# Optimization experiments

Hardware: AMD Instinct MI355X
Metric: run time of the kernel (lower is better)

Reference implementation:

```python
import jax, jax.numpy as jnp
import numpy as np

DN = ('NCHW', 'OIHW', 'NCHW')
NUM_DOMAINS = 4


def conv2d(x, w, pad, groups=1):
    return jax.lax.conv_general_dilated(x, w, (1, 1), pad, dimension_numbers=DN,
                                        feature_group_count=groups)


def batchnorm2d(x, w, b, eps=1e-3):
    m = x.mean(axis=(0, 2, 3), keepdims=True)
    v = x.var(axis=(0, 2, 3), keepdims=True)
    return (x - m) / jnp.sqrt(v + eps) * w[None, :, None, None] + b[None, :, None, None]


def avgpool_w(x, k):
    B, C, H, W = x.shape
    Wo = W // k
    return x[..., :Wo * k].reshape(B, C, H, Wo, k).mean(axis=-1)


def mink(u, v):
    # Minkowski inner product <u,v>_L = -u0*v0 + <us,vs>
    return -u[..., 0] * v[..., 0] + (u[..., 1:] * v[..., 1:]).sum(-1)


def lorentz_elu(x):
    s = jax.nn.elu(x[..., 1:])
    t = jnp.sqrt(1.0 + (s * s).sum(-1, keepdims=True))
    return jnp.concatenate([t, s], -1)


def lorentz_avgpool_w(x, k):
    # (B,H,W,C) Lorentz points; window mean then Lorentz centroid projection
    B, H, W, C = x.shape
    Wo = W // k
    s = x[:, :, :Wo * k].reshape(B, H, Wo, k, C).mean(axis=3)
    d = jnp.sqrt(jnp.clip(jnp.abs(mink(s, s)), 1e-8, None))[..., None]
    return s / d


def lorentz_dbn(x, domains, beta, gamma, eps=1e-5):
    # Domain-specific Riemannian batch norm on the Lorentz manifold (k=1),
    # scalar dispersion (Frechet-mean centroid + geodesic variance per domain).
    B, H, W, C = x.shape
    pts = x.reshape(B, H * W, C)
    npts = float(H * W)
    s = jax.ops.segment_sum(pts.sum(axis=1), domains, num_segments=NUM_DOMAINS)  # (D,C)
    cnt = jax.ops.segment_sum(jnp.full((B,), npts, x.dtype), domains, num_segments=NUM_DOMAINS)
    cnt = jnp.maximum(cnt, 1.0)
    s = s / cnt[:, None]
    mu = s / jnp.sqrt(jnp.clip(jnp.abs(mink(s, s)), 1e-8, None))[:, None]  # (D,C) centroids
    mu_b = mu[domains][:, None, :]                                         # (B,1,C)
    ip = mink(mu_b, pts)                                                   # (B,HW)
    dist = jnp.arccosh(jnp.clip(-ip, 1.0 + 1e-7, None))
    u = pts + ip[..., None] * mu_b
    un = jnp.sqrt(jnp.clip(mink(u, u), 1e-8, None))
    v = dist[..., None] * u / un[..., None]                                # log_mu(x)
    var = jax.ops.segment_sum((dist ** 2).sum(axis=1), domains, num_segments=NUM_DOMAINS) / cnt
    o = jnp.zeros((C,), x.dtype).at[0].set(1.0)
    # parallel transport mu -> origin
    v = v + (-v[..., :1]) / (1.0 + mu_b[..., :1]) * (mu_b + o)
    # rescale by gamma / sqrt(var)
    v = v * (gamma / jnp.sqrt(var[domains] + eps))[:, None, None]
    # parallel transport origin -> beta, then expmap at beta
    v = v + (mink(beta, v) / (1.0 + beta[0]))[..., None] * (o + beta)
    vn = jnp.sqrt(jnp.clip(mink(v, v), 1e-8, None))[..., None]
    y = jnp.cosh(vn) * beta + jnp.sinh(vn) * v / vn
    return y.reshape(B, H, W, C)


def setup_inputs() -> dict:
    key = jax.random.key(0)
    ks = jax.random.split(key, 12)
    B = 128
    d = {}
    d['x'] = jax.random.normal(ks[0], (B, 32, 1024), jnp.float32)
    d['domains'] = jax.random.randint(ks[1], (B,), 0, NUM_DOMAINS, jnp.int32)
    d['conv1_w'] = 0.1 * jax.random.normal(ks[2], (16, 1, 1, 32), jnp.float32)
    d['bn1_w'] = jnp.ones((16,), jnp.float32)
    d['bn1_b'] = jnp.zeros((16,), jnp.float32)
    d['dw_w'] = 0.1 * jax.random.normal(ks[3], (32, 1, 32, 1), jnp.float32)
    d['bn2_w'] = jnp.ones((32,), jnp.float32)
    d['bn2_b'] = jnp.zeros((32,), jnp.float32)
    d['ec1_w'] = 0.1 * jax.random.normal(ks[4], (32, 1, 1, 16), jnp.float32)
    d['b2c1_w'] = 0.1 * jax.random.normal(ks[5], (32, 1, 1, 16), jnp.float32)
    d['b2c2_w'] = 0.1 * jax.random.normal(ks[6], (32, 32, 1, 1), jnp.float32)
    d['bn3_w'] = jnp.ones((32,), jnp.float32)
    d['bn3_b'] = jnp.zeros((32,), jnp.float32)
    d['lc1_w'] = 0.2 * jax.random.normal(ks[7], (33, 33), jnp.float32)
    d['bn_beta'] = jnp.zeros((33,), jnp.float32).at[0].set(1.0)
    d['bn_gamma'] = jnp.ones((1,), jnp.float32)
    d['mlr_a'] = 0.1 * jax.random.normal(ks[8], (1,), jnp.float32)
    d['mlr_z'] = 0.1 * jax.random.normal(ks[9], (1, 512), jnp.float32)
    return d


def reference(x, domains, conv1_w, bn1_w, bn1_b, dw_w, bn2_w, bn2_b, ec1_w,
              b2c1_w, b2c2_w, bn3_w, bn3_b, lc1_w, bn_beta, bn_gamma, mlr_a, mlr_z):
    h = x[:, None]                                       # (B,1,32,1024)
    # block1: temporal conv + BN + depthwise spatial conv + BN + ELU + pool
    h = conv2d(h, conv1_w, ((0, 0), (16, 16)))           # (B,16,32,1025)
    h = batchnorm2d(h, bn1_w, bn1_b)
    h = conv2d(h, dw_w, ((0, 0), (0, 0)), groups=16)     # (B,32,1,1025)
    h = batchnorm2d(h, bn2_w, bn2_b)
    h = jax.nn.elu(h)
    h = avgpool_w(h, 4)                                  # (B,32,1,256)
    # ec1 + block2
    h = conv2d(h, ec1_w, ((0, 0), (8, 8)), groups=32)    # (B,32,1,257)
    h = conv2d(h, b2c1_w, ((0, 0), (8, 8)), groups=32)   # (B,32,1,258)
    h = conv2d(h, b2c2_w, ((0, 0), (0, 0)))              # (B,32,1,258)
    h = batchnorm2d(h, bn3_w, bn3_b)
    h = jax.nn.elu(h)
    h = avgpool_w(h, 4)                                  # (B,32,1,64)
    # to Lorentz: permute, L2-normalize, pad time, projx (time = sqrt(1+|s|^2))
    h = jnp.transpose(h, (0, 2, 3, 1))                   # (B,1,64,32)
    h = h / jnp.clip(jnp.linalg.norm(h, axis=-1, keepdims=True), 1e-12, None)
    t = jnp.sqrt(1.0 + (h * h).sum(-1, keepdims=True))
    h = jnp.concatenate([t, h], -1)                      # (B,1,64,33)
    # LorentzConv2d kernel 1 == Lorentz fully-connected: linear then recompute time
    y = jnp.einsum('bhwc,oc->bhwo', h, lc1_w)
    ys = y[..., 1:]
    yt = jnp.sqrt(1.0 + (ys * ys).sum(-1, keepdims=True))
    h = jnp.concatenate([yt, ys], -1)                    # (B,1,64,33)
    h = lorentz_dbn(h, domains, bn_beta, bn_gamma)
    h = lorentz_elu(h)
    h = lorentz_avgpool_w(h, 4)                          # (B,1,16,33)
    # lorentz_flatten: concat spaces, recompute time -> (B, 16*32+1)
    B = h.shape[0]
    fs = h[..., 1:].reshape(B, -1)
    ft = jnp.sqrt(1.0 + (fs * fs).sum(-1, keepdims=True))
    features = jnp.concatenate([ft, fs], -1)             # (B,513)
    # Lorentz MLR (k=1)
    norm_z = jnp.linalg.norm(mlr_z, axis=-1)             # (1,)
    w_t = jnp.sinh(mlr_a) * norm_z
    bet = jnp.sqrt(jnp.clip(-w_t ** 2 + (jnp.cosh(mlr_a) * norm_z) ** 2, 1e-8, None))
    alpha = -w_t * features[:, :1] + jnp.cosh(mlr_a) * (features[:, 1:] @ mlr_z.T)
    dd = jnp.abs(jnp.arcsinh(alpha / bet))
    logits = jnp.sign(alpha) * bet * dd                  # (B,1)
    return logits.squeeze(-1), features
```

## Files before the change

### kernel.cpp

```cpp
#include <hip/hip_runtime.h>
#include <math.h>

#define Bn 128
#define Hh 32
#define Wx 1024

#define N1f 4198400.0f
#define N2f 131200.0f
#define N3f 33024.0f

#define OFF_EH     33
#define OFF_ET     48
#define OFF_G      64
#define OFF_G2     544
#define OFF_A1     1024
#define OFF_B1     1040
#define OFF_S1_3   1056
#define OFF_S2_3   1088
#define OFF_SEG    1120
#define OFF_CNT    1252
#define OFF_DSQ    1256
#define ZERO_N     1280
#define OFF_PC     2048
#define OFF_PS     34816
#define OFF_PD1    35840
#define OFF_PD2    68608
#define OFF_DWOUT  101376
#define OFF_E2     (101376 + 4194304)
#define OFF_C3     OFF_DWOUT
#define OFF_PTS    (OFF_C3 + 1056768)
#define OFF_VO     (OFF_PTS + 270336)

__device__ __forceinline__ float eluf(float x) { return x > 0.f ? x : expm1f(x); }

__global__ __launch_bounds__(256) void k_edge(const float* __restrict__ x,
                                              float* __restrict__ ws) {
    __shared__ float hd[64 * 48];
    __shared__ float tl[64 * 48];
    int tid = threadIdx.x;
    int r0 = blockIdx.x * 64;
    for (int i = tid; i < 64 * 32; i += 256) {
        int r = i >> 5, c = i & 31;
        tl[r * 48 + 16 + c] = 0.f;
    }
#pragma unroll
    for (int it = 0; it < 4; it++) {
        int idx = tid + it * 256;
        int r = idx >> 4, q = idx & 15;
        const float4* base = (const float4*)(x + (r0 + r) * Wx);
        if (q < 12) ((float4*)(hd + r * 48))[q] = base[q];
        else        ((float4*)(tl + r * 48))[q - 12] = base[252 + (q - 12)];
    }
    __syncthreads();
    for (int p = tid; p < 990; p += 256) {
        float acc = 0.f;
        if (p < 480) {
            int d = p / 15, j = p - d * 15;
            for (int r = 0; r < 64; r++) acc += hd[r * 48 + j] * hd[r * 48 + j + d];
            atomicAdd(&ws[OFF_G + p], acc);
        } else if (p < 960) {
            int p2 = p - 480;
            int d = p2 / 15, j = p2 - d * 15;
            for (int r = 0; r < 64; r++) acc += tl[r * 48 + 1 + j] * tl[r * 48 + 1 + j + d];
            atomicAdd(&ws[OFF_G2 + p2], acc);
        } else {
            int j = p - 960;
            if (j < 15) { for (int r = 0; r < 64; r++) acc += hd[r * 48 + j]; }
            else        { for (int r = 0; r < 64; r++) acc += tl[r * 48 + 1 + (j - 15)]; }
            atomicAdd(&ws[OFF_EH + j], acc);
        }
    }
}

__global__ __launch_bounds__(256, 1) void k_corr(const float* __restrict__ x,
                                                 float* __restrict__ ws) {
    __shared__ float xs[2][1060];
    __shared__ float cacc[32];
    __shared__ float sacc;
    int tid = threadIdx.x;
    if (tid < 32) cacc[tid] = 0.f;
    if (tid == 32) sacc = 0.f;
    for (int i = 1024 + tid; i < 1060; i += 256) { xs[0][i] = 0.f; xs[1][i] = 0.f; }
    float acc[32];
#pragma unroll
    for (int d = 0; d < 32; d++) acc[d] = 0.f;
    float sp = 0.f;
    int r0 = blockIdx.x * 4;
    ((float4*)xs[0])[tid] = ((const float4*)(x + r0 * Wx))[tid];
    __syncthreads();
    for (int rr = 0; rr < 4; rr++) {
        float4 nxt;
        if (rr < 3) nxt = ((const float4*)(x + (r0 + rr + 1) * Wx))[tid];
        const float* bq = xs[rr & 1];
        float v[36];
#pragma unroll
        for (int q = 0; q < 9; q++) {
            float4 t4 = ((const float4*)bq)[tid + q];
            v[4 * q] = t4.x; v[4 * q + 1] = t4.y; v[4 * q + 2] = t4.z; v[4 * q + 3] = t4.w;
        }
#pragma unroll
        for (int i = 0; i < 4; i++) {
            sp += v[i];
#pragma unroll
            for (int d = 0; d < 32; d++) acc[d] += v[i] * v[i + d];
        }
        if (rr < 3) ((float4*)xs[(rr + 1) & 1])[tid] = nxt;
        __syncthreads();
    }
    int lane = tid & 63;
#pragma unroll
    for (int d = 0; d < 32; d++) {
        float vv = acc[d];
#pragma unroll
        for (int off = 32; off > 0; off >>= 1) vv += __shfl_down(vv, off);
        if (lane == 0) atomicAdd(&cacc[d], vv);
    }
    {
        float vv = sp;
#pragma unroll
        for (int off = 32; off > 0; off >>= 1) vv += __shfl_down(vv, off);
        if (lane == 0) atomicAdd(&sacc, vv);
    }
    __syncthreads();
    if (tid < 32) ws[OFF_PC + tid * 1024 + blockIdx.x] = cacc[tid];
    if (tid == 32) ws[OFF_PS + blockIdx.x] = sacc;
}

__global__ __launch_bounds__(512) void k_fold(const float* __restrict__ w1,
                                              const float* __restrict__ bn1w,
                                              const float* __restrict__ bn1b,
                                              float* __restrict__ ws) {
    __shared__ float PH[32][16];
    __shared__ float PT[32][16];
    __shared__ float Ts[32];
    __shared__ float w1s[512];
    __shared__ float sumsq[16];
    __shared__ float meanv[16];
    __shared__ float Cs[32];
    __shared__ float sS[16];
    int tid = threadIdx.x;
    w1s[tid] = w1[tid];
    if (tid < 16) sumsq[tid] = 0.f;
    {
        int d = tid >> 4, i = tid & 15;
        const float4* pc = (const float4*)(ws + OFF_PC + d * 1024 + i * 64);
        float s = 0.f;
#pragma unroll
        for (int k = 0; k < 16; k++) { float4 t4 = pc[k]; s += t4.x + t4.y + t4.z + t4.w; }
        s += __shfl_down(s, 8); s += __shfl_down(s, 4);
        s += __shfl_down(s, 2); s += __shfl_down(s, 1);
        if (i == 0) Cs[d] = s;
    }
    __syncthreads();
    if (tid < 32) {
        int d = tid;
        float s = 0.f;
        for (int j = 0; j < 15; j++) { s += ws[OFF_G + d * 15 + j]; PH[d][j] = s; }
        float s2 = 0.f;
        for (int j = 14; j >= 0; j--) { s2 += ws[OFF_G2 + d * 15 + j]; PT[d][j] = s2; }
    } else if (tid < 48) {
        int i = tid - 32;
        const float4* ps = (const float4*)(ws + OFF_PS + i * 64);
        float s = 0.f;
#pragma unroll
        for (int k = 0; k < 16; k++) { float4 t4 = ps[k]; s += t4.x + t4.y + t4.z + t4.w; }
        sS[i] = s;
    }
    __syncthreads();
    if (tid >= 64 && tid < 96) {
        int k = tid - 64;
        float S = 0.f;
        for (int j = 0; j < 16; j++) S += sS[j];
        float t = S;
        for (int j = 0; j <= k - 17; j++) t -= ws[OFF_EH + j];
        if (k <= 14) for (int j = k; j < 15; j++) t -= ws[OFF_ET + j];
        Ts[k] = t;
    }
    __syncthreads();
    int c = tid >> 5, d = tid & 31;
    float Cd = Cs[d];
    float part = 0.f;
    for (int k = 0; k + d < 32; k++) {
        float head = (k >= 17) ? PH[d][k - 17] : 0.f;
        float tail = (k <= 14) ? PT[d][k] : 0.f;
        float R = Cd - head - tail;
        part += w1s[c * 32 + k] * w1s[c * 32 + k + d] * R;
    }
    if (d > 0) part *= 2.f;
    atomicAdd(&sumsq[c], part);
    if (d == 0) {
        float mp = 0.f;
        for (int k = 0; k < 32; k++) mp += w1s[c * 32 + k] * Ts[k];
        meanv[c] = mp / N1f;
    }
    __syncthreads();
    if (tid < 16) {
        float mean = meanv[tid];
        float var = fmaxf(sumsq[tid] / N1f - mean * mean, 0.f);
        float a = bn1w[tid] / sqrtf(var + 1e-3f);
        ws[OFF_A1 + tid] = a;
        ws[OFF_B1 + tid] = bn1b[tid] - mean * a;
    }
}

__global__ __launch_bounds__(256, 2) void k_dw(const float* __restrict__ x,
                                               const float* __restrict__ w1,
                                               const float* __restrict__ dww,
                                               float* __restrict__ ws) {
    __shared__ float buf[32 * 160];
    __shared__ float dws[1024];
    __shared__ float w1s[512];
    __shared__ float a1s[16], b1s[16], Dv[32];
    int tid = threadIdx.x;
    int b = blockIdx.x;
    int z = blockIdx.y;
    int wt0 = z * 128;
    for (int i = tid; i < 1024; i += 256) dws[i] = dww[i];
    w1s[tid] = w1[tid];
    w1s[256 + tid] = w1[256 + tid];
    if (tid < 16) { a1s[tid] = ws[OFF_A1 + tid]; b1s[tid] = ws[OFF_B1 + tid]; }
    const float* xb = x + b * (Hh * Wx);
    for (int i = tid; i < 32 * 160; i += 256) {
        int h = i / 160, cc = i - h * 160;
        int gc = wt0 - 16 + cc;
        buf[i] = (gc >= 0 && gc < Wx) ? xb[h * Wx + gc] : 0.f;
    }
    __syncthreads();
    if (tid < 32) {
        float d = 0.f;
        for (int h = 0; h < 32; h++) d += dws[tid * 32 + h];
        Dv[tid] = d;
    }
    float acc[32];
    if (tid < 160) {
        float xv[32];
#pragma unroll
        for (int h = 0; h < 32; h++) xv[h] = buf[h * 160 + tid];
#pragma unroll
        for (int oc = 0; oc < 32; oc++) acc[oc] = 0.f;
#pragma unroll
        for (int h = 0; h < 32; h++) {
#pragma unroll
            for (int oc = 0; oc < 32; oc++) acc[oc] += xv[h] * dws[oc * 32 + h];
        }
    }
    __syncthreads();
    if (tid < 160) {
#pragma unroll
        for (int oc = 0; oc < 32; oc++) buf[oc * 160 + tid] = acc[oc];
    }
    __syncthreads();
    int lane = tid & 63;
    int wave = tid >> 6;
    int half = lane >> 5;
    int qw = lane & 31;
    for (int pass = 0; pass < 4; pass++) {
        int oc = pass * 8 + wave * 2 + half;
        int g = oc >> 1;
        float wr[32];
        const float4* wg = (const float4*)(w1s + g * 32);
#pragma unroll
        for (int q = 0; q < 8; q++) {
            float4 t4 = wg[q];
            wr[4 * q] = t4.x; wr[4 * q + 1] = t4.y; wr[4 * q + 2] = t4.z; wr[4 * q + 3] = t4.w;
        }
        float ag = a1s[g], bb = b1s[g] * Dv[oc];
        float y[36];
        const float4* yq = (const float4*)(buf + oc * 160 + 4 * qw);
#pragma unroll
        for (int q = 0; q < 9; q++) {
            float4 t4 = yq[q];
            y[4 * q] = t4.x; y[4 * q + 1] = t4.y; y[4 * q + 2] = t4.z; y[4 * q + 3] = t4.w;
        }
        float ls1 = 0.f, ls2 = 0.f;
        float ov[4];
#pragma unroll
        for (int m = 0; m < 4; m++) {
            float s = 0.f;
#pragma unroll
            for (int k = 0; k < 32; k++) s += wr[k] * y[m + k];
            float val = ag * s + bb;
            ov[m] = val;
            ls1 += val; ls2 += val * val;
        }
        *((float4*)(ws + OFF_DWOUT + (b * 32 + oc) * 1024 + wt0 + 4 * qw)) =
            make_float4(ov[0], ov[1], ov[2], ov[3]);
        if (z == 7 && qw == 0) {
            float s = 0.f;
#pragma unroll
            for (int k = 0; k < 32; k++) s += wr[k] * buf[oc * 160 + 128 + k];
            float val = ag * s + bb;
            ls1 += val; ls2 += val * val;
        }
#pragma unroll
        for (int off = 16; off > 0; off >>= 1) {
            ls1 += __shfl_down(ls1, off, 32);
            ls2 += __shfl_down(ls2, off, 32);
        }
        if (qw == 0) {
            ws[OFF_PD1 + oc * 1024 + z * 128 + b] = ls1;
            ws[OFF_PD2 + oc * 1024 + z * 128 + b] = ls2;
        }
    }
}

__global__ __launch_bounds__(64) void k_pe(const float* __restrict__ ec1w,
                                           const float* __restrict__ bc1w,
                                           const float* __restrict__ bn2w,
                                           const float* __restrict__ bn2b,
                                           float* __restrict__ ws) {
    __shared__ float ins[272];
    __shared__ float e1p[288];
    int b = blockIdx.x, c = blockIdx.y;
    int t = threadIdx.x;
    if (t < 8) { ins[t] = 0.f; ins[264 + t] = 0.f; e1p[t] = 0.f; }
    if (t < 23) e1p[265 + t] = 0.f;
    const float4* p1 = (const float4*)(ws + OFF_PD1 + c * 1024);
    const float4* p2 = (const float4*)(ws + OFF_PD2 + c * 1024);
    float s1 = 0.f, s2 = 0.f;
#pragma unroll
    for (int q = 0; q < 4; q++) {
        float4 a4 = p1[t * 4 + q];
        float4 c4 = p2[t * 4 + q];
        s1 += a4.x + a4.y + a4.z + a4.w;
        s2 += c4.x + c4.y + c4.z + c4.w;
    }
#pragma unroll
    for (int off = 32; off > 0; off >>= 1) {
        s1 += __shfl_xor(s1, off);
        s2 += __shfl_xor(s2, off);
    }
    float mean = s1 / N2f;
    float var = fmaxf(s2 / N2f - mean * mean, 0.f);
    float a = bn2w[c] / sqrtf(var + 1e-3f);
    float bb = bn2b[c] - mean * a;
    const float4* dr = (const float4*)(ws + OFF_DWOUT + (b * 32 + c) * 1024);
#pragma unroll
    for (int q = 0; q < 4; q++) {
        float4 v4 = dr[q * 64 + t];
        ins[8 + q * 64 + t] = 0.25f * (eluf(a * v4.x + bb) + eluf(a * v4.y + bb) +
                                       eluf(a * v4.z + bb) + eluf(a * v4.w + bb));
    }
    __syncthreads();
    float ek[16], bk[16];
#pragma unroll
    for (int k = 0; k < 16; k++) { ek[k] = ec1w[c * 16 + k]; bk[k] = bc1w[c * 16 + k]; }
    for (int w = t; w < 257; w += 64) {
        float s = 0.f;
#pragma unroll
        for (int k = 0; k < 16; k++) s += ins[w + k] * ek[k];
        e1p[8 + w] = s;
    }
    __syncthreads();
    float* e2r = ws + OFF_E2 + (b * 32 + c) * 258;
    for (int w = t; w < 258; w += 64) {
        float s = 0.f;
#pragma unroll
        for (int k = 0; k < 16; k++) s += e1p[w + k] * bk[k];
        e2r[w] = s;
    }
}

__global__ __launch_bounds__(256) void k_sep2(const float* __restrict__ bc2w,
                                              float* __restrict__ ws) {
    __shared__ float es[32 * 129];
    __shared__ float bs[1056];
    int b = blockIdx.x;
    int wb = blockIdx.y * 129;
    int t = threadIdx.x;
    for (int i = t; i < 1024; i += 256) { int o = i >> 5, cc = i & 31; bs[o * 33 + cc] = bc2w[i]; }
    const float* e2b = ws + OFF_E2 + b * 8256;
    for (int i = t; i < 4128; i += 256) {
        int cc = i / 129, wl = i - cc * 129;
        es[i] = e2b[cc * 258 + wb + wl];
    }
    __syncthreads();
    int o = t >> 3, w0 = t & 7;
    float wr[32];
#pragma unroll
    for (int cc = 0; cc < 32; cc++) wr[cc] = bs[o * 33 + cc];
    float s1 = 0.f, s2 = 0.f;
    float* c3r = ws + OFF_C3 + (b * 32 + o) * 258 + wb;
    for (int wl = w0; wl < 129; wl += 8) {
        float s = 0.f;
#pragma unroll
        for (int cc = 0; cc < 32; cc++) s += es[cc * 129 + wl] * wr[cc];
        c3r[wl] = s;
        s1 += s; s2 += s * s;
    }
    s1 += __shfl_down(s1, 4, 8); s1 += __shfl_down(s1, 2, 8); s1 += __shfl_down(s1, 1, 8);
    s2 += __shfl_down(s2, 4, 8); s2 += __shfl_down(s2, 2, 8); s2 += __shfl_down(s2, 1, 8);
    if (w0 == 0) {
        atomicAdd(&ws[OFF_S1_3 + o], s1);
        atomicAdd(&ws[OFF_S2_3 + o], s2);
    }
}

__global__ __launch_bounds__(256, 1) void k_head(const float* __restrict__ bn3w,
                                                 const float* __restrict__ bn3b,
                                                 const float* __restrict__ lc1w,
                                                 const int* __restrict__ domains,
                                                 float* __restrict__ ws) {
    __shared__ float q[2048];
    __shared__ float lc1s[1089];
    __shared__ float psum[33];
    __shared__ float ssyp[4][64];
    __shared__ float a3s[32], b3s[32];
    int tid = threadIdx.x;
    int b = blockIdx.x;
    if (tid < 32) {
        float mean = ws[OFF_S1_3 + tid] / N3f;
        float var = fmaxf(ws[OFF_S2_3 + tid] / N3f - mean * mean, 0.f);
        float a = bn3w[tid] / sqrtf(var + 1e-3f);
        a3s[tid] = a;
        b3s[tid] = bn3b[tid] - mean * a;
    }
    for (int i = tid; i < 1089; i += 256) lc1s[i] = lc1w[i];
    __syncthreads();
    const float* c3 = ws + OFF_C3 + b * 8256;
    for (int idx = tid; idx < 2048; idx += 256) {
        int c = idx >> 6, wp = idx & 63;
        float a = a3s[c], bb = b3s[c];
        float acc = 0.f;
#pragma unroll
        for (int j = 0; j < 4; j++) {
            float e = a * c3[c * 258 + wp * 4 + j] + bb;
            acc += eluf(e);
        }
        q[idx] = 0.25f * acc;
    }
    __syncthreads();
    int w = tid & 63, sub = tid >> 6;
    float qv[32];
    float ssq = 0.f;
#pragma unroll
    for (int c = 0; c < 32; c++) { qv[c] = q[c * 64 + w]; ssq += qv[c] * qv[c]; }
    float inv = 1.f / fmaxf(sqrtf(ssq), 1e-12f);
    float ss2 = 0.f;
#pragma unroll
    for (int c = 0; c < 32; c++) { qv[c] *= inv; ss2 += qv[c] * qv[c]; }
    float t = sqrtf(1.f + ss2);
    int o0 = 1 + sub * 8;
    float p[8];
    float ssy_part = 0.f;
#pragma unroll
    for (int i = 0; i < 8; i++) {
        int o = o0 + i;
        float s = lc1s[o * 33] * t;
#pragma unroll
        for (int c = 0; c < 32; c++) s += lc1s[o * 33 + 1 + c] * qv[c];
        p[i] = s;
        ssy_part += s * s;
    }
    ssyp[sub][w] = ssy_part;
    float* pr = ws + OFF_PTS + (b * 64 + w) * 33;
#pragma unroll
    for (int i = 0; i < 8; i++) pr[o0 + i] = p[i];
    __syncthreads();
    float yt = 0.f;
    if (sub == 0) {
        float ssy = ssyp[0][w] + ssyp[1][w] + ssyp[2][w] + ssyp[3][w];
        yt = sqrtf(1.f + ssy);
        pr[0] = yt;
    }
#pragma unroll
    for (int i = 0; i < 8; i++) {
        float vv = p[i];
#pragma unroll
        for (int off = 32; off > 0; off >>= 1) vv += __shfl_down(vv, off);
        if (w == 0) psum[o0 + i] = vv;
    }
    {
        float vv = yt;
#pragma unroll
        for (int off = 32; off > 0; off >>= 1) vv += __shfl_down(vv, off);
        if (w == 0 && sub == 0) psum[0] = vv;
    }
    __syncthreads();
    int dom = domains[b];
    if (tid < 33) atomicAdd(&ws[OFF_SEG + dom * 33 + tid], psum[tid]);
    if (tid == 64) atomicAdd(&ws[OFF_CNT + dom], 64.f);
}

__global__ __launch_bounds__(64, 1) void k_tangent(const int* __restrict__ domains,
                                                   float* __restrict__ ws) {
    int b = blockIdx.x;
    int w = threadIdx.x;
    int dom = domains[b];
    float cnt = fmaxf(ws[OFF_CNT + dom], 1.f);
    float m[33];
    float s0 = ws[OFF_SEG + dom * 33] / cnt;
    m[0] = s0;
    float msum = 0.f;
#pragma unroll
    for (int c = 1; c < 33; c++) {
        m[c] = ws[OFF_SEG + dom * 33 + c] / cnt;
        msum += m[c] * m[c];
    }
    float mkm = -s0 * s0 + msum;
    float dn = 1.f / sqrtf(fmaxf(fabsf(mkm), 1e-8f));
#pragma unroll
    for (int c = 0; c < 33; c++) m[c] *= dn;
    const float* pr = ws + OFF_PTS + (b * 64 + w) * 33;
    float p[33];
#pragma unroll
    for (int c = 0; c < 33; c++) p[c] = pr[c];
    float ip = -m[0] * p[0];
#pragma unroll
    for (int c = 1; c < 33; c++) ip += m[c] * p[c];
    float z = fmaxf(-ip, 1.f + 1e-7f);
    float dist = acoshf(z);
    float u[33];
#pragma unroll
    for (int c = 0; c < 33; c++) u[c] = p[c] + ip * m[c];
    float mk = -u[0] * u[0];
#pragma unroll
    for (int c = 1; c < 33; c++) mk += u[c] * u[c];
    float un = sqrtf(fmaxf(mk, 1e-8f));
    float r = dist / un;
    float v0 = r * u[0];
    float coef = -v0 / (1.f + m[0]);
    float* vo = ws + OFF_VO + (b * 64 + w) * 33;
    vo[0] = v0 + coef * (m[0] + 1.f);
#pragma unroll
    for (int c = 1; c < 33; c++) vo[c] = r * u[c] + coef * m[c];
    float dsq = dist * dist;
#pragma unroll
    for (int off = 32; off > 0; off >>= 1) dsq += __shfl_down(dsq, off);
    if (w == 0) atomicAdd(&ws[OFF_DSQ + dom], dsq);
}

__global__ __launch_bounds__(64, 1) void k_final(const int* __restrict__ domains,
                                                 const float* __restrict__ beta,
                                                 const float* __restrict__ gamma,
                                                 const float* __restrict__ mlr_a,
                                                 const float* __restrict__ mlr_z,
                                                 float* __restrict__ ws,
                                                 float* __restrict__ out) {
    __shared__ float he[64 * 33];
    __shared__ float hp[16 * 33];
    int b = blockIdx.x;
    int w = threadIdx.x;
    int dom = domains[b];
    float cnt = fmaxf(ws[OFF_CNT + dom], 1.f);
    float var = ws[OFF_DSQ + dom] / cnt;
    float sc = gamma[0] / sqrtf(var + 1e-5f);
    float bt[33];
#pragma unroll
    for (int c = 0; c < 33; c++) bt[c] = beta[c];
    const float* vo = ws + OFF_VO + (b * 64 + w) * 33;
    float v[33];
#pragma unroll
    for (int c = 0; c < 33; c++) v[c] = vo[c] * sc;
    float mb = -bt[0] * v[0];
#pragma unroll
    for (int c = 1; c < 33; c++) mb += bt[c] * v[c];
    float coef = mb / (1.f + bt[0]);
    v[0] += coef * (1.f + bt[0]);
#pragma unroll
    for (int c = 1; c < 33; c++) v[c] += coef * bt[c];
    float mk = -v[0] * v[0];
#pragma unroll
    for (int c = 1; c < 33; c++) mk += v[c] * v[c];
    float vn = sqrtf(fmaxf(mk, 1e-8f));
    float ch = coshf(vn), sh = sinhf(vn) / vn;
    float ss = 0.f;
#pragma unroll
    for (int c = 1; c < 33; c++) {
        float y = ch * bt[c] + sh * v[c];
        float s = eluf(y);
        he[w * 33 + c] = s;
        ss += s * s;
    }
    he[w * 33] = sqrtf(1.f + ss);
    __syncthreads();
    if (w < 16) {
        float tmp[33];
        float mk2;
        {
            float a0 = 0.25f * (he[(4 * w) * 33] + he[(4 * w + 1) * 33] +
                                he[(4 * w + 2) * 33] + he[(4 * w + 3) * 33]);
            tmp[0] = a0;
            mk2 = -a0 * a0;
        }
#pragma unroll
        for (int c = 1; c < 33; c++) {
            float a = 0.25f * (he[(4 * w) * 33 + c] + he[(4 * w + 1) * 33 + c] +
                               he[(4 * w + 2) * 33 + c] + he[(4 * w + 3) * 33 + c]);
            tmp[c] = a;
            mk2 += a * a;
        }
        float dd = sqrtf(fmaxf(fabsf(mk2), 1e-8f));
#pragma unroll
        for (int c = 0; c < 33; c++) hp[w * 33 + c] = tmp[c] / dd;
    }
    __syncthreads();
    float ssq = 0.f, sdz = 0.f, zz = 0.f;
    for (int j = w; j < 512; j += 64) {
        float val = hp[(j >> 5) * 33 + 1 + (j & 31)];
        float zv = mlr_z[j];
        ssq += val * val;
        sdz += val * zv;
        zz += zv * zv;
        out[128 + b * 513 + 1 + j] = val;
    }
#pragma unroll
    for (int off = 32; off > 0; off >>= 1) {
        ssq += __shfl_down(ssq, off);
        sdz += __shfl_down(sdz, off);
        zz += __shfl_down(zz, off);
    }
    if (w == 0) {
        float nz = sqrtf(zz);
        float a = mlr_a[0];
        float cha = coshf(a);
        float wt = sinhf(a) * nz;
        float cn = cha * nz;
        float bet = sqrtf(fmaxf(cn * cn - wt * wt, 1e-8f));
        float ft = sqrtf(1.f + ssq);
        float alpha = -wt * ft + cha * sdz;
        out[128 + b * 513] = ft;
        out[b] = bet * asinhf(alpha / bet);
    }
}

extern "C" void kernel_launch(void* const* d_in, const int* in_sizes, int n_in,
                              void* d_out, int out_size, void* d_ws, size_t ws_size,
                              hipStream_t stream) {
    const float* x       = (const float*)d_in[0];
    const int*   domains = (const int*)d_in[1];
    const float* conv1_w = (const float*)d_in[2];
    const float* bn1_w   = (const float*)d_in[3];
    const float* bn1_b   = (const float*)d_in[4];
    const float* dw_w    = (const float*)d_in[5];
    const float* bn2_w   = (const float*)d_in[6];
    const float* bn2_b   = (const float*)d_in[7];
    const float* ec1_w   = (const float*)d_in[8];
    const float* b2c1_w  = (const float*)d_in[9];
    const float* b2c2_w  = (const float*)d_in[10];
    const float* bn3_w   = (const float*)d_in[11];
    const float* bn3_b   = (const float*)d_in[12];
    const float* lc1_w   = (const float*)d_in[13];
    const float* bn_beta = (const float*)d_in[14];
    const float* bn_gamma= (const float*)d_in[15];
    const float* mlr_a   = (const float*)d_in[16];
    const float* mlr_z   = (const float*)d_in[17];
    float* out = (float*)d_out;
    float* ws  = (float*)d_ws;

    hipMemsetAsync(ws, 0, ZERO_N * sizeof(float), stream);
    k_edge<<<64, 256, 0, stream>>>(x, ws);
    k_corr<<<1024, 256, 0, stream>>>(x, ws);
    k_fold<<<1, 512, 0, stream>>>(conv1_w, bn1_w, bn1_b, ws);
    k_dw<<<dim3(128, 8), 256, 0, stream>>>(x, conv1_w, dw_w, ws);
    k_pe<<<dim3(128, 32), 64, 0, stream>>>(ec1_w, b2c1_w, bn2_w, bn2_b, ws);
    k_sep2<<<dim3(128, 2), 256, 0, stream>>>(b2c2_w, ws);
    k_head<<<Bn, 256, 0, stream>>>(bn3_w, bn3_b, lc1_w, domains, ws);
    k_tangent<<<Bn, 64, 0, stream>>>(domains, ws);
    k_final<<<Bn, 64, 0, stream>>>(domains, bn_beta, bn_gamma, mlr_a, mlr_z, ws, out);
}
```

Before: 248.6 us.

## Widen k_dw width tile to 256 and read weights directly from global

The depthwise-conv kernel now covers 256 output columns per block instead of 128, halving the grid and shrinking the 16-column halo overhead. Weight tiles are no longer staged in shared memory but read as uniform float4 loads from global. Each wave handles a full 64-lane row per output channel, so the partial-sum layout shrinks and k_pe reads half as many partials. In exchange there are fewer blocks in flight and more shared memory per block, which may lower occupancy.

```diff
diff --git a/kernel.cpp b/kernel.cpp
--- a/kernel.cpp
+++ b/kernel.cpp
@@ -24,9 +24,9 @@
 #define OFF_PC     2048
 #define OFF_PS     34816
 #define OFF_PD1    35840
-#define OFF_PD2    68608
-#define OFF_DWOUT  101376
-#define OFF_E2     (101376 + 4194304)
+#define OFF_PD2    52224
+#define OFF_DWOUT  68608
+#define OFF_E2     (68608 + 4194304)
 #define OFF_C3     OFF_DWOUT
 #define OFF_PTS    (OFF_C3 + 1056768)
 #define OFF_VO     (OFF_PTS + 270336)
@@ -207,66 +207,64 @@
                                                const float* __restrict__ w1,
                                                const float* __restrict__ dww,
                                                float* __restrict__ ws) {
-    __shared__ float buf[32 * 160];
-    __shared__ float dws[1024];
-    __shared__ float w1s[512];
+    __shared__ float buf[32 * 288];
     __shared__ float a1s[16], b1s[16], Dv[32];
     int tid = threadIdx.x;
     int b = blockIdx.x;
     int z = blockIdx.y;
-    int wt0 = z * 128;
-    for (int i = tid; i < 1024; i += 256) dws[i] = dww[i];
-    w1s[tid] = w1[tid];
-    w1s[256 + tid] = w1[256 + tid];
+    int wt0 = z * 256;
     if (tid < 16) { a1s[tid] = ws[OFF_A1 + tid]; b1s[tid] = ws[OFF_B1 + tid]; }
+    else if (tid >= 32 && tid < 64) {
+        int oc = tid - 32;
+        float d = 0.f;
+        for (int h = 0; h < 32; h++) d += dww[oc * 32 + h];
+        Dv[oc] = d;
+    }
     const float* xb = x + b * (Hh * Wx);
-    for (int i = tid; i < 32 * 160; i += 256) {
-        int h = i / 160, cc = i - h * 160;
+    for (int i = tid; i < 32 * 288; i += 256) {
+        int h = i / 288, cc = i - h * 288;
         int gc = wt0 - 16 + cc;
         buf[i] = (gc >= 0 && gc < Wx) ? xb[h * Wx + gc] : 0.f;
     }
     __syncthreads();
-    if (tid < 32) {
-        float d = 0.f;
-        for (int h = 0; h < 32; h++) d += dws[tid * 32 + h];
-        Dv[tid] = d;
-    }
-    float acc[32];
-    if (tid < 160) {
+    for (int rep = 0; rep < 2; rep++) {
+        if (rep == 1 && tid >= 32) break;
+        int c = rep == 0 ? tid : 256 + tid;
         float xv[32];
 #pragma unroll
-        for (int h = 0; h < 32; h++) xv[h] = buf[h * 160 + tid];
-#pragma unroll
-        for (int oc = 0; oc < 32; oc++) acc[oc] = 0.f;
-#pragma unroll
-        for (int h = 0; h < 32; h++) {
-#pragma unroll
-            for (int oc = 0; oc < 32; oc++) acc[oc] += xv[h] * dws[oc * 32 + h];
-        }
-    }
-    __syncthreads();
-    if (tid < 160) {
-#pragma unroll
-        for (int oc = 0; oc < 32; oc++) buf[oc * 160 + tid] = acc[oc];
+        for (int h = 0; h < 32; h++) xv[h] = buf[h * 288 + c];
+        float acc[32];
+#pragma unroll
+        for (int oc = 0; oc < 32; oc++) {
+            const float4* dg = (const float4*)(dww + oc * 32);
+            float a = 0.f;
+#pragma unroll
+            for (int hq = 0; hq < 8; hq++) {
+                float4 d = dg[hq];
+                a += xv[4 * hq] * d.x + xv[4 * hq + 1] * d.y +
+                     xv[4 * hq + 2] * d.z + xv[4 * hq + 3] * d.w;
+            }
+            acc[oc] = a;
+        }
+#pragma unroll
+        for (int oc = 0; oc < 32; oc++) buf[oc * 288 + c] = acc[oc];
     }
     __syncthreads();
     int lane = tid & 63;
-    int wave = tid >> 6;
-    int half = lane >> 5;
-    int qw = lane & 31;
-    for (int pass = 0; pass < 4; pass++) {
-        int oc = pass * 8 + wave * 2 + half;
+    int wv = __builtin_amdgcn_readfirstlane(tid >> 6);
+    for (int pass = 0; pass < 8; pass++) {
+        int oc = pass * 4 + wv;
         int g = oc >> 1;
+        const float4* wg4 = (const float4*)(w1 + g * 32);
         float wr[32];
-        const float4* wg = (const float4*)(w1s + g * 32);
 #pragma unroll
         for (int q = 0; q < 8; q++) {
-            float4 t4 = wg[q];
+            float4 t4 = wg4[q];
             wr[4 * q] = t4.x; wr[4 * q + 1] = t4.y; wr[4 * q + 2] = t4.z; wr[4 * q + 3] = t4.w;
         }
         float ag = a1s[g], bb = b1s[g] * Dv[oc];
         float y[36];
-        const float4* yq = (const float4*)(buf + oc * 160 + 4 * qw);
+        const float4* yq = (const float4*)(buf + oc * 288 + 4 * lane);
 #pragma unroll
         for (int q = 0; q < 9; q++) {
             float4 t4 = yq[q];
@@ -283,23 +281,23 @@
             ov[m] = val;
             ls1 += val; ls2 += val * val;
         }
-        *((float4*)(ws + OFF_DWOUT + (b * 32 + oc) * 1024 + wt0 + 4 * qw)) =
+        *((float4*)(ws + OFF_DWOUT + (b * 32 + oc) * 1024 + wt0 + 4 * lane)) =
             make_float4(ov[0], ov[1], ov[2], ov[3]);
-        if (z == 7 && qw == 0) {
+        if (z == 3 && lane == 0) {
             float s = 0.f;
 #pragma unroll
-            for (int k = 0; k < 32; k++) s += wr[k] * buf[oc * 160 + 128 + k];
+            for (int k = 0; k < 32; k++) s += wr[k] * buf[oc * 288 + 256 + k];
             float val = ag * s + bb;
             ls1 += val; ls2 += val * val;
         }
 #pragma unroll
-        for (int off = 16; off > 0; off >>= 1) {
-            ls1 += __shfl_down(ls1, off, 32);
-            ls2 += __shfl_down(ls2, off, 32);
-        }
-        if (qw == 0) {
-            ws[OFF_PD1 + oc * 1024 + z * 128 + b] = ls1;
-            ws[OFF_PD2 + oc * 1024 + z * 128 + b] = ls2;
+        for (int off = 32; off > 0; off >>= 1) {
+            ls1 += __shfl_down(ls1, off);
+            ls2 += __shfl_down(ls2, off);
+        }
+        if (lane == 0) {
+            ws[OFF_PD1 + oc * 512 + z * 128 + b] = ls1;
+            ws[OFF_PD2 + oc * 512 + z * 128 + b] = ls2;
         }
     }
 }
@@ -315,16 +313,11 @@
     int t = threadIdx.x;
     if (t < 8) { ins[t] = 0.f; ins[264 + t] = 0.f; e1p[t] = 0.f; }
     if (t < 23) e1p[265 + t] = 0.f;
-    const float4* p1 = (const float4*)(ws + OFF_PD1 + c * 1024);
-    const float4* p2 = (const float4*)(ws + OFF_PD2 + c * 1024);
-    float s1 = 0.f, s2 = 0.f;
-#pragma unroll
-    for (int q = 0; q < 4; q++) {
-        float4 a4 = p1[t * 4 + q];
-        float4 c4 = p2[t * 4 + q];
-        s1 += a4.x + a4.y + a4.z + a4.w;
-        s2 += c4.x + c4.y + c4.z + c4.w;
-    }
+    const float4* p1 = (const float4*)(ws + OFF_PD1 + c * 512);
+    const float4* p2 = (const float4*)(ws + OFF_PD2 + c * 512);
+    float4 a0 = p1[t * 2], a1 = p1[t * 2 + 1], c0 = p2[t * 2], c1 = p2[t * 2 + 1];
+    float s1 = a0.x + a0.y + a0.z + a0.w + a1.x + a1.y + a1.z + a1.w;
+    float s2 = c0.x + c0.y + c0.z + c0.w + c1.x + c1.y + c1.z + c1.w;
 #pragma unroll
     for (int off = 32; off > 0; off >>= 1) {
         s1 += __shfl_xor(s1, off);
@@ -652,7 +645,7 @@
     k_edge<<<64, 256, 0, stream>>>(x, ws);
     k_corr<<<1024, 256, 0, stream>>>(x, ws);
     k_fold<<<1, 512, 0, stream>>>(conv1_w, bn1_w, bn1_b, ws);
-    k_dw<<<dim3(128, 8), 256, 0, stream>>>(x, conv1_w, dw_w, ws);
+    k_dw<<<dim3(128, 4), 256, 0, stream>>>(x, conv1_w, dw_w, ws);
     k_pe<<<dim3(128, 32), 64, 0, stream>>>(ec1_w, b2c1_w, bn2_w, bn2_b, ws);
     k_sep2<<<dim3(128, 2), 256, 0, stream>>>(b2c2_w, ws);
     k_head<<<Bn, 256, 0, stream>>>(bn3_w, bn3_b, lc1_w, domains, ws);
```

New measurement: 240.1 us. -3.4%, faster.

## Fuse pooled separable conv stages into one per-batch kernel, drop atomics

Applied to the files above, without the earlier changes.

Merges k_pe and k_sep2 into one kernel per batch item that keeps the intermediate e2 tensor in shared memory instead of writing it to global memory and reading it back. The BN3 statistics atomics are replaced by per-batch partial sums that k_head reduces itself. k_dw now loads x straight from global into registers, skipping the shared staging buffer and one barrier. The trade-off is that only 128 blocks run the fused stage instead of 4096 plus 256, which lowers parallelism and adds extra barriers per channel pass.

```diff
diff --git a/kernel.cpp b/kernel.cpp
--- a/kernel.cpp
+++ b/kernel.cpp
@@ -15,8 +15,6 @@
 #define OFF_G2     544
 #define OFF_A1     1024
 #define OFF_B1     1040
-#define OFF_S1_3   1056
-#define OFF_S2_3   1088
 #define OFF_SEG    1120
 #define OFF_CNT    1252
 #define OFF_DSQ    1256
@@ -25,9 +23,9 @@
 #define OFF_PS     34816
 #define OFF_PD1    35840
 #define OFF_PD2    68608
-#define OFF_DWOUT  101376
-#define OFF_E2     (101376 + 4194304)
-#define OFF_C3     OFF_DWOUT
+#define OFF_PB3    101376
+#define OFF_DWOUT  109568
+#define OFF_C3     (109568 + 4194304)
 #define OFF_PTS    (OFF_C3 + 1056768)
 #define OFF_VO     (OFF_PTS + 270336)
 
@@ -219,33 +217,32 @@
     w1s[tid] = w1[tid];
     w1s[256 + tid] = w1[256 + tid];
     if (tid < 16) { a1s[tid] = ws[OFF_A1 + tid]; b1s[tid] = ws[OFF_B1 + tid]; }
-    const float* xb = x + b * (Hh * Wx);
-    for (int i = tid; i < 32 * 160; i += 256) {
-        int h = i / 160, cc = i - h * 160;
-        int gc = wt0 - 16 + cc;
-        buf[i] = (gc >= 0 && gc < Wx) ? xb[h * Wx + gc] : 0.f;
-    }
     __syncthreads();
     if (tid < 32) {
         float d = 0.f;
         for (int h = 0; h < 32; h++) d += dws[tid * 32 + h];
         Dv[tid] = d;
     }
-    float acc[32];
     if (tid < 160) {
+        int gc = wt0 - 16 + tid;
+        bool inr = (gc >= 0 && gc < Wx);
+        const float* xb = x + b * (Hh * Wx) + gc;
         float xv[32];
 #pragma unroll
-        for (int h = 0; h < 32; h++) xv[h] = buf[h * 160 + tid];
-#pragma unroll
-        for (int oc = 0; oc < 32; oc++) acc[oc] = 0.f;
-#pragma unroll
-        for (int h = 0; h < 32; h++) {
-#pragma unroll
-            for (int oc = 0; oc < 32; oc++) acc[oc] += xv[h] * dws[oc * 32 + h];
-        }
-    }
-    __syncthreads();
-    if (tid < 160) {
+        for (int h = 0; h < 32; h++) xv[h] = inr ? xb[h << 10] : 0.f;
+        float acc[32];
+#pragma unroll
+        for (int oc = 0; oc < 32; oc++) {
+            const float4* dg = (const float4*)(dws + oc * 32);
+            float a = 0.f;
+#pragma unroll
+            for (int hq = 0; hq < 8; hq++) {
+                float4 d = dg[hq];
+                a += xv[4 * hq] * d.x + xv[4 * hq + 1] * d.y +
+                     xv[4 * hq + 2] * d.z + xv[4 * hq + 3] * d.w;
+            }
+            acc[oc] = a;
+        }
 #pragma unroll
         for (int oc = 0; oc < 32; oc++) buf[oc * 160 + tid] = acc[oc];
     }
@@ -304,95 +301,95 @@
     }
 }
 
-__global__ __launch_bounds__(64) void k_pe(const float* __restrict__ ec1w,
-                                           const float* __restrict__ bc1w,
-                                           const float* __restrict__ bn2w,
-                                           const float* __restrict__ bn2b,
-                                           float* __restrict__ ws) {
-    __shared__ float ins[272];
-    __shared__ float e1p[288];
-    int b = blockIdx.x, c = blockIdx.y;
+__global__ __launch_bounds__(256) void k_pesep(const float* __restrict__ ec1w,
+                                               const float* __restrict__ bc1w,
+                                               const float* __restrict__ bn2w,
+                                               const float* __restrict__ bn2b,
+                                               const float* __restrict__ bc2w,
+                                               float* __restrict__ ws) {
+    __shared__ float e2s[32 * 258];
+    __shared__ float ins[4][272];
+    __shared__ float e1p[4][288];
+    __shared__ float bs[1056];
+    __shared__ float a2s[32], b2s[32];
+    int b = blockIdx.x;
     int t = threadIdx.x;
-    if (t < 8) { ins[t] = 0.f; ins[264 + t] = 0.f; e1p[t] = 0.f; }
-    if (t < 23) e1p[265 + t] = 0.f;
-    const float4* p1 = (const float4*)(ws + OFF_PD1 + c * 1024);
-    const float4* p2 = (const float4*)(ws + OFF_PD2 + c * 1024);
-    float s1 = 0.f, s2 = 0.f;
-#pragma unroll
-    for (int q = 0; q < 4; q++) {
-        float4 a4 = p1[t * 4 + q];
-        float4 c4 = p2[t * 4 + q];
-        s1 += a4.x + a4.y + a4.z + a4.w;
-        s2 += c4.x + c4.y + c4.z + c4.w;
-    }
-#pragma unroll
-    for (int off = 32; off > 0; off >>= 1) {
-        s1 += __shfl_xor(s1, off);
-        s2 += __shfl_xor(s2, off);
-    }
-    float mean = s1 / N2f;
-    float var = fmaxf(s2 / N2f - mean * mean, 0.f);
-    float a = bn2w[c] / sqrtf(var + 1e-3f);
-    float bb = bn2b[c] - mean * a;
-    const float4* dr = (const float4*)(ws + OFF_DWOUT + (b * 32 + c) * 1024);
-#pragma unroll
-    for (int q = 0; q < 4; q++) {
-        float4 v4 = dr[q * 64 + t];
-        ins[8 + q * 64 + t] = 0.25f * (eluf(a * v4.x + bb) + eluf(a * v4.y + bb) +
-                                       eluf(a * v4.z + bb) + eluf(a * v4.w + bb));
-    }
-    __syncthreads();
-    float ek[16], bk[16];
-#pragma unroll
-    for (int k = 0; k < 16; k++) { ek[k] = ec1w[c * 16 + k]; bk[k] = bc1w[c * 16 + k]; }
-    for (int w = t; w < 257; w += 64) {
-        float s = 0.f;
-#pragma unroll
-        for (int k = 0; k < 16; k++) s += ins[w + k] * ek[k];
-        e1p[8 + w] = s;
-    }
-    __syncthreads();
-    float* e2r = ws + OFF_E2 + (b * 32 + c) * 258;
-    for (int w = t; w < 258; w += 64) {
-        float s = 0.f;
-#pragma unroll
-        for (int k = 0; k < 16; k++) s += e1p[w + k] * bk[k];
-        e2r[w] = s;
-    }
-}
-
-__global__ __launch_bounds__(256) void k_sep2(const float* __restrict__ bc2w,
-                                              float* __restrict__ ws) {
-    __shared__ float es[32 * 129];
-    __shared__ float bs[1056];
-    int b = blockIdx.x;
-    int wb = blockIdx.y * 129;
-    int t = threadIdx.x;
+    int wave = t >> 6, lane = t & 63;
     for (int i = t; i < 1024; i += 256) { int o = i >> 5, cc = i & 31; bs[o * 33 + cc] = bc2w[i]; }
-    const float* e2b = ws + OFF_E2 + b * 8256;
-    for (int i = t; i < 4128; i += 256) {
-        int cc = i / 129, wl = i - cc * 129;
-        es[i] = e2b[cc * 258 + wb + wl];
-    }
-    __syncthreads();
+    {
+        int c = t >> 3, i = t & 7;
+        const float4* p1 = (const float4*)(ws + OFF_PD1 + c * 1024 + i * 128);
+        const float4* p2 = (const float4*)(ws + OFF_PD2 + c * 1024 + i * 128);
+        float s1 = 0.f, s2 = 0.f;
+#pragma unroll
+        for (int q = 0; q < 32; q++) {
+            float4 a4 = p1[q]; s1 += a4.x + a4.y + a4.z + a4.w;
+            float4 c4 = p2[q]; s2 += c4.x + c4.y + c4.z + c4.w;
+        }
+        s1 += __shfl_down(s1, 4, 8); s1 += __shfl_down(s1, 2, 8); s1 += __shfl_down(s1, 1, 8);
+        s2 += __shfl_down(s2, 4, 8); s2 += __shfl_down(s2, 2, 8); s2 += __shfl_down(s2, 1, 8);
+        if (i == 0) {
+            float mean = s1 / N2f;
+            float var = fmaxf(s2 / N2f - mean * mean, 0.f);
+            float a = bn2w[c] / sqrtf(var + 1e-3f);
+            a2s[c] = a;
+            b2s[c] = bn2b[c] - mean * a;
+        }
+    }
+    if (lane < 8) { ins[wave][lane] = 0.f; ins[wave][264 + lane] = 0.f; e1p[wave][lane] = 0.f; }
+    if (lane < 23) e1p[wave][265 + lane] = 0.f;
+    __syncthreads();
+    for (int pass = 0; pass < 8; pass++) {
+        int c = pass * 4 + wave;
+        float a = a2s[c], bb = b2s[c];
+        const float4* dr = (const float4*)(ws + OFF_DWOUT + (b * 32 + c) * 1024);
+#pragma unroll
+        for (int q = 0; q < 4; q++) {
+            float4 v4 = dr[q * 64 + lane];
+            ins[wave][8 + q * 64 + lane] = 0.25f * (eluf(a * v4.x + bb) + eluf(a * v4.y + bb) +
+                                                    eluf(a * v4.z + bb) + eluf(a * v4.w + bb));
+        }
+        __syncthreads();
+        float ek[16], bk[16];
+#pragma unroll
+        for (int k = 0; k < 16; k++) { ek[k] = ec1w[c * 16 + k]; bk[k] = bc1w[c * 16 + k]; }
+        for (int w = lane; w < 257; w += 64) {
+            float s = 0.f;
+#pragma unroll
+            for (int k = 0; k < 16; k++) s += ins[wave][w + k] * ek[k];
+            e1p[wave][8 + w] = s;
+        }
+        __syncthreads();
+        for (int w = lane; w < 258; w += 64) {
+            float s = 0.f;
+#pragma unroll
+            for (int k = 0; k < 16; k++) s += e1p[wave][w + k] * bk[k];
+            e2s[c * 258 + w] = s;
+        }
+        __syncthreads();
+    }
     int o = t >> 3, w0 = t & 7;
     float wr[32];
 #pragma unroll
     for (int cc = 0; cc < 32; cc++) wr[cc] = bs[o * 33 + cc];
     float s1 = 0.f, s2 = 0.f;
-    float* c3r = ws + OFF_C3 + (b * 32 + o) * 258 + wb;
-    for (int wl = w0; wl < 129; wl += 8) {
-        float s = 0.f;
-#pragma unroll
-        for (int cc = 0; cc < 32; cc++) s += es[cc * 129 + wl] * wr[cc];
-        c3r[wl] = s;
-        s1 += s; s2 += s * s;
+#pragma unroll
+    for (int half = 0; half < 2; half++) {
+        int wb = half * 129;
+        float* c3r = ws + OFF_C3 + (b * 32 + o) * 258 + wb;
+        for (int wl = w0; wl < 129; wl += 8) {
+            float s = 0.f;
+#pragma unroll
+            for (int cc = 0; cc < 32; cc++) s += e2s[cc * 258 + wb + wl] * wr[cc];
+            c3r[wl] = s;
+            s1 += s; s2 += s * s;
+        }
     }
     s1 += __shfl_down(s1, 4, 8); s1 += __shfl_down(s1, 2, 8); s1 += __shfl_down(s1, 1, 8);
     s2 += __shfl_down(s2, 4, 8); s2 += __shfl_down(s2, 2, 8); s2 += __shfl_down(s2, 1, 8);
     if (w0 == 0) {
-        atomicAdd(&ws[OFF_S1_3 + o], s1);
-        atomicAdd(&ws[OFF_S2_3 + o], s2);
+        ws[OFF_PB3 + b * 32 + o] = s1;
+        ws[OFF_PB3 + 4096 + b * 32 + o] = s2;
     }
 }
 
@@ -409,8 +406,13 @@
     int tid = threadIdx.x;
     int b = blockIdx.x;
     if (tid < 32) {
-        float mean = ws[OFF_S1_3 + tid] / N3f;
-        float var = fmaxf(ws[OFF_S2_3 + tid] / N3f - mean * mean, 0.f);
+        float s1 = 0.f, s2 = 0.f;
+        for (int bb2 = 0; bb2 < 128; bb2++) {
+            s1 += ws[OFF_PB3 + bb2 * 32 + tid];
+            s2 += ws[OFF_PB3 + 4096 + bb2 * 32 + tid];
+        }
+        float mean = s1 / N3f;
+        float var = fmaxf(s2 / N3f - mean * mean, 0.f);
         float a = bn3w[tid] / sqrtf(var + 1e-3f);
         a3s[tid] = a;
         b3s[tid] = bn3b[tid] - mean * a;
@@ -653,8 +655,7 @@
     k_corr<<<1024, 256, 0, stream>>>(x, ws);
     k_fold<<<1, 512, 0, stream>>>(conv1_w, bn1_w, bn1_b, ws);
     k_dw<<<dim3(128, 8), 256, 0, stream>>>(x, conv1_w, dw_w, ws);
-    k_pe<<<dim3(128, 32), 64, 0, stream>>>(ec1_w, b2c1_w, bn2_w, bn2_b, ws);
-    k_sep2<<<dim3(128, 2), 256, 0, stream>>>(b2c2_w, ws);
+    k_pesep<<<Bn, 256, 0, stream>>>(ec1_w, b2c1_w, bn2_w, bn2_b, b2c2_w, ws);
     k_head<<<Bn, 256, 0, stream>>>(bn3_w, bn3_b, lc1_w, domains, ws);
     k_tangent<<<Bn, 64, 0, stream>>>(domains, ws);
     k_final<<<Bn, 64, 0, stream>>>(domains, bn_beta, bn_gamma, mlr_a, mlr_z, ws, out);
```

New measurement: 251.8 us. About the same (+1.3%).
